# Optimization experiments

Measured on AMD Instinct MI355X. Metric: run time of the kernel, lower is better.

Reference implementation:

```python
import jax, jax.numpy as jnp
import numpy as np

F_DIM = 256
DFF = 2048      # torch TransformerEncoderLayer default dim_feedforward
NHEAD = 4
NCLS = 7
MAXLEN = 256
BATCH = 256
LN_EPS = 1e-5


def _layer_norm(x, g, b):
    m = x.mean(-1, keepdims=True)
    v = ((x - m) ** 2).mean(-1, keepdims=True)
    return (x - m) / jnp.sqrt(v + LN_EPS) * g + b


def _pos_encoding(n, d):
    # NOTE: original code builds PE over x.size(1) (the batch dim) -- kept faithfully.
    pos = jnp.arange(n, dtype=jnp.float32)[:, None]
    div = jnp.exp(jnp.arange(0, d, 2, dtype=jnp.float32) * (-np.log(10000.0) / d))
    pe = jnp.zeros((n, d), dtype=jnp.float32)
    pe = pe.at[:, 0::2].set(jnp.sin(pos * div))
    pe = pe.at[:, 1::2].set(jnp.cos(pos * div))
    return pe


def _mha(x, Wqkv, bqkv, Wo, bo):
    # x: [S, B, F]  (torch MHA default seq-first layout)
    S, B, F = x.shape
    hd = F // NHEAD
    qkv = x @ Wqkv.T + bqkv                      # [S, B, 3F]
    q, k, v = jnp.split(qkv, 3, axis=-1)
    rs = lambda t: t.reshape(S, B, NHEAD, hd).transpose(1, 2, 0, 3)  # [B, h, S, hd]
    q, k, v = rs(q), rs(k), rs(v)
    attn = jax.nn.softmax(jnp.einsum('bhsd,bhtd->bhst', q, k) / jnp.float32(np.sqrt(hd)), axis=-1)
    o = jnp.einsum('bhst,bhtd->bhsd', attn, v).transpose(2, 0, 1, 3).reshape(S, B, F)
    return o @ Wo.T + bo


def _forward(U_s, U_p, W_emb, b_emb, Wqkv, bqkv, Wo, bo, ln1_g, ln1_b,
             W1, b1, W2, b2, ln2_g, ln2_b, W_fc, b_fc, W_sm, b_sm, seq_lengths):
    L = np.asarray(seq_lengths)                   # static host lengths
    T, B, F = U_s.shape
    mask = jnp.arange(T)[:, None] < jnp.asarray(L)[None, :]        # [T, B] valid-turn mask
    bank_s = U_s * mask[:, :, None]               # zero-padded, as feature_transfer does
    # ---- ReasonMod / MultiTurnTransformer (post-LN encoder layer, eval mode) ----
    h = bank_s @ W_emb.T + b_emb
    h = h + _pos_encoding(B, F)                   # faithful quirk: PE over batch dim
    a_out = _mha(h, Wqkv, bqkv, Wo, bo)
    h1 = _layer_norm(h + a_out, ln1_g, ln1_b)
    ff = jax.nn.relu(h1 @ W1.T + b1) @ W2.T + b2
    h2 = _layer_norm(h1 + ff, ln2_g, ln2_b)
    q = h + h2                                    # [T, B, F]; identical for every t in the loop
    # ---- gather + segment-softmax + scatter-add attention pooling, all t at once ----
    e = jnp.einsum('ibf,tbf->tib', U_p, q)        # scores per (target t, turn i, conv b)
    e = jnp.where(mask[None, :, :], e, -1e30)
    a = jax.nn.softmax(e, axis=1) * mask[None, :, :]
    r = jnp.einsum('tib,ibf->tbf', a, U_p * mask[:, :, None])      # scatter_add equivalent
    rc = jnp.concatenate([bank_s, r], axis=-1)    # [T, B, 2F]
    hidden = jax.nn.relu(rc @ W_fc.T + b_fc)
    logp = jax.nn.log_softmax(hidden @ W_sm.T + b_sm, axis=2)      # [T, B, n_classes]
    rows = np.concatenate([np.arange(l) for l in L])
    cols = np.repeat(np.arange(B), L)
    return logp[rows, cols]                       # [total_tokens, n_classes]


def setup_inputs() -> dict:
    key = jax.random.key(0)
    ks = jax.random.split(key, 24)
    rn = lambda k, shape, s=0.05: jax.random.normal(k, shape, dtype=jnp.float32) * s
    F, D2 = F_DIM, 2 * F_DIM
    inp = {
        'U_s': jax.random.normal(ks[0], (MAXLEN, BATCH, F), dtype=jnp.float32),
        'U_p': jax.random.normal(ks[1], (MAXLEN, BATCH, F), dtype=jnp.float32),
        'W_emb': rn(ks[2], (F, F)), 'b_emb': jnp.zeros((F,), jnp.float32),
        'Wqkv': rn(ks[3], (3 * F, F)), 'bqkv': jnp.zeros((3 * F,), jnp.float32),
        'Wo': rn(ks[4], (F, F)), 'bo': jnp.zeros((F,), jnp.float32),
        'ln1_g': jnp.ones((F,), jnp.float32), 'ln1_b': jnp.zeros((F,), jnp.float32),
        'W1': rn(ks[5], (DFF, F)), 'b1': jnp.zeros((DFF,), jnp.float32),
        'W2': rn(ks[6], (F, DFF)), 'b2': jnp.zeros((F,), jnp.float32),
        'ln2_g': jnp.ones((F,), jnp.float32), 'ln2_b': jnp.zeros((F,), jnp.float32),
        'W_fc': rn(ks[7], (D2, D2)), 'b_fc': jnp.zeros((D2,), jnp.float32),
        'W_sm': rn(ks[8], (NCLS, D2)), 'b_sm': jnp.zeros((NCLS,), jnp.float32),
        'seq_lengths': jax.random.randint(ks[9], (BATCH,), MAXLEN // 2, MAXLEN + 1),
    }
    return inp


def reference(U_s, U_p, W_emb, b_emb, Wqkv, bqkv, Wo, bo, ln1_g, ln1_b,
              W1, b1, W2, b2, ln2_g, ln2_b, W_fc, b_fc, W_sm, b_sm, seq_lengths):
    return _forward(U_s, U_p, W_emb, b_emb, Wqkv, bqkv, Wo, bo, ln1_g, ln1_b,
                    W1, b1, W2, b2, ln2_g, ln2_b, W_fc, b_fc, W_sm, b_sm, seq_lengths)
```

## Files before the change

### kernel.cpp

```cpp
#include <hip/hip_runtime.h>

#define MTB 65536

typedef unsigned int uint;
typedef unsigned short ushort;

typedef _Float16 h8 __attribute__((ext_vector_type(8)));
typedef __attribute__((ext_vector_type(4))) float f4;

enum { E_BIAS=1, E_RELU=2, E_ACC=4, E_RES=8, E_PE=16, E_MASKA=32 };

__device__ __forceinline__ float ldsc(const float* p) { return *p; }
__device__ __forceinline__ float ldsc(const _Float16* p) { return (float)*p; }

template<int EPI, int AMODE, int BMODE, typename CT, int CPL, typename RT, int RPL>
__global__ __launch_bounds__(256) void gemm_h(
    int M, int N, int K,
    const void* __restrict__ Ap, const void* __restrict__ Ap2, int lda, long batchA,
    const void* __restrict__ Bp, int ldw, long batchW,
    CT* __restrict__ C, long cplane, int ldc, long batchC,
    const float* __restrict__ bias,
    const RT* __restrict__ res, const RT* __restrict__ resLo,
    const float* __restrict__ pe,
    const int* __restrict__ seqlen)
{
    __shared__ _Float16 Ah[128][40];
    __shared__ _Float16 Al[(AMODE==3)?128:1][40];
    __shared__ _Float16 Bh[128][40];
    __shared__ _Float16 Bl[(BMODE==0)?128:1][40];

    const int z = blockIdx.z;
    C += (size_t)z * batchC;
    const float*    Af  = (const float*)Ap + (AMODE==0 ? (size_t)z*batchA : 0);
    const _Float16* Ahp = (const _Float16*)Ap + ((AMODE==2||AMODE==3) ? (size_t)z*batchA : 0);
    const _Float16* Alp = (const _Float16*)Ap2 + (AMODE==3 ? (size_t)z*batchA : 0);
    const float*    Bf  = (const float*)Bp + (BMODE!=2 ? (size_t)z*batchW : 0);
    const _Float16* Bhp = (const _Float16*)Bp;

    const int m0 = blockIdx.y * 128, n0 = blockIdx.x * 128;
    const int tid = threadIdx.x;
    const int lane = tid & 63, wid = tid >> 6;
    const int wr = wid >> 1, wc = wid & 1;

    f4 acc[4][4];
    {
        f4 zr = {0.f, 0.f, 0.f, 0.f};
        #pragma unroll
        for (int i = 0; i < 4; i++)
            #pragma unroll
            for (int j = 0; j < 4; j++) acc[i][j] = zr;
    }

    for (int k0 = 0; k0 < K; k0 += 32) {
        __syncthreads();
        if (AMODE == 0 || (AMODE == 4 && k0 < 256)) {
            #pragma unroll
            for (int i = 0; i < 4; i++) {
                const int row = i*32 + (tid>>3);
                const int cg  = (tid&7)<<2;
                const int m = m0 + row;
                float4 v; v.x=0.f; v.y=0.f; v.z=0.f; v.w=0.f;
                bool ok = true;
                if (EPI & E_MASKA) ok = ((m>>8) < seqlen[m&255]);
                if (ok) v = *(const float4*)(Af + (size_t)m*lda + k0 + cg);
                Ah[row][cg+0] = (_Float16)v.x;
                Ah[row][cg+1] = (_Float16)v.y;
                Ah[row][cg+2] = (_Float16)v.z;
                Ah[row][cg+3] = (_Float16)v.w;
            }
        } else if (AMODE == 4) {
            const _Float16* Ar = (const _Float16*)Ap2;
            const int row = tid >> 1;
            const int cg  = (tid & 1) << 4;
            const size_t off = (size_t)(m0 + row) * 256 + (k0 - 256) + cg;
            *(uint4*)&Ah[row][cg]     = *(const uint4*)(Ar + off);
            *(uint4*)&Ah[row][cg + 8] = *(const uint4*)(Ar + off + 8);
        } else {
            const int row = tid >> 1;
            const int cg  = (tid & 1) << 4;
            const size_t off = (size_t)(m0 + row) * lda + k0 + cg;
            *(uint4*)&Ah[row][cg]     = *(const uint4*)(Ahp + off);
            *(uint4*)&Ah[row][cg + 8] = *(const uint4*)(Ahp + off + 8);
            if (AMODE == 3) {
                *(uint4*)&Al[row][cg]     = *(const uint4*)(Alp + off);
                *(uint4*)&Al[row][cg + 8] = *(const uint4*)(Alp + off + 8);
            }
        }
        if (BMODE == 2) {
            const int row = tid >> 1;
            const int cg  = (tid & 1) << 4;
            const size_t off = (size_t)(n0 + row) * ldw + k0 + cg;
            *(uint4*)&Bh[row][cg]     = *(const uint4*)(Bhp + off);
            *(uint4*)&Bh[row][cg + 8] = *(const uint4*)(Bhp + off + 8);
        } else if (BMODE == 0) {
            #pragma unroll
            for (int i = 0; i < 4; i++) {
                const int row = i*32 + (tid>>3);
                const int cg  = (tid&7)<<2;
                float4 v = *(const float4*)(Bf + (size_t)(n0+row)*ldw + k0 + cg);
                _Float16 h0 = (_Float16)v.x, h1 = (_Float16)v.y,
                         h2 = (_Float16)v.z, h3 = (_Float16)v.w;
                Bh[row][cg+0]=h0; Bl[row][cg+0]=(_Float16)(v.x-(float)h0);
                Bh[row][cg+1]=h1; Bl[row][cg+1]=(_Float16)(v.y-(float)h1);
                Bh[row][cg+2]=h2; Bl[row][cg+2]=(_Float16)(v.z-(float)h2);
                Bh[row][cg+3]=h3; Bl[row][cg+3]=(_Float16)(v.w-(float)h3);
            }
        } else {
            #pragma unroll
            for (int i = 0; i < 4; i++) {
                const int kr = i*8 + (tid>>5);
                const int ng = (tid&31)<<2;
                float4 v = *(const float4*)(Bf + (size_t)(k0+kr)*ldw + n0 + ng);
                Bh[ng+0][kr] = (_Float16)v.x;
                Bh[ng+1][kr] = (_Float16)v.y;
                Bh[ng+2][kr] = (_Float16)v.z;
                Bh[ng+3][kr] = (_Float16)v.w;
            }
        }
        __syncthreads();
        const int lr = lane & 15, lk = (lane>>4)<<3;
        h8 ah[4], bh[4];
        #pragma unroll
        for (int i = 0; i < 4; i++) {
            ah[i] = *(const h8*)&Ah[wr*64 + i*16 + lr][lk];
            bh[i] = *(const h8*)&Bh[wc*64 + i*16 + lr][lk];
        }
        #pragma unroll
        for (int mi = 0; mi < 4; mi++)
            #pragma unroll
            for (int ni = 0; ni < 4; ni++)
                acc[mi][ni] = __builtin_amdgcn_mfma_f32_16x16x32_f16(ah[mi], bh[ni], acc[mi][ni], 0, 0, 0);
        if (AMODE == 3) {
            h8 al[4], bl[4];
            #pragma unroll
            for (int i = 0; i < 4; i++) {
                al[i] = *(const h8*)&Al[wr*64 + i*16 + lr][lk];
                bl[i] = *(const h8*)&Bl[wc*64 + i*16 + lr][lk];
            }
            #pragma unroll
            for (int mi = 0; mi < 4; mi++)
                #pragma unroll
                for (int ni = 0; ni < 4; ni++) {
                    acc[mi][ni] = __builtin_amdgcn_mfma_f32_16x16x32_f16(ah[mi], bl[ni], acc[mi][ni], 0, 0, 0);
                    acc[mi][ni] = __builtin_amdgcn_mfma_f32_16x16x32_f16(al[mi], bh[ni], acc[mi][ni], 0, 0, 0);
                }
        }
    }
    const int colb = n0 + wc*64;
    const int rowb = m0 + wr*64;
    #pragma unroll
    for (int ni = 0; ni < 4; ni++) {
        const int col = colb + ni*16 + (lane & 15);
        float bv = (EPI & E_BIAS) ? bias[col] : 0.f;
        #pragma unroll
        for (int mi = 0; mi < 4; mi++) {
            const int r0 = rowb + mi*16 + ((lane>>4)<<2);
            #pragma unroll
            for (int j = 0; j < 4; j++) {
                const int row = r0 + j;
                const size_t idx = (size_t)row*ldc + col;
                float v = acc[mi][ni][j] + bv;
                if (EPI & E_PE)  v += pe[((row & 255) << 8) + col];
                if (EPI & E_RES) {
                    v += ldsc(res + idx);
                    if (RPL) v += ldsc(resLo + idx);
                }
                CT* cp = C + idx;
                if (EPI & E_ACC) v += ldsc((const CT*)cp);
                if (EPI & E_RELU) v = fmaxf(v, 0.f);
                if (CPL) {
                    _Float16 hh = (_Float16)v;
                    *(_Float16*)cp = hh;
                    *((_Float16*)cp + cplane) = (_Float16)(v - (float)hh);
                } else if (sizeof(CT) == 2) {
                    *(_Float16*)cp = (_Float16)v;
                } else {
                    *(float*)cp = v;
                }
            }
        }
    }
}

__global__ __launch_bounds__(256) void ff_kernel(
    const _Float16* __restrict__ h1,
    const _Float16* __restrict__ W1p,
    const _Float16* __restrict__ W2p,
    const float* __restrict__ b1,
    const float* __restrict__ b2,
    float* __restrict__ res2)
{
    __shared__ _Float16 h1t[64][264];
    __shared__ _Float16 zt[64][136];
    __shared__ _Float16 Bs[256][40];
    const int m0 = blockIdx.x * 64;
    const int tid = threadIdx.x;
    const int lane = tid & 63, wid = tid >> 6;
    const int wr = wid >> 1, wc = wid & 1;
    const int lr = lane & 15, lk = (lane >> 4) << 3;
    const int l4 = (lane >> 4) << 2;

    {
        const int row = tid >> 2, c0 = (tid & 3) << 6;
        const _Float16* src = h1 + (size_t)(m0 + row) * 256 + c0;
        #pragma unroll
        for (int j = 0; j < 8; j++)
            *(uint4*)&h1t[row][c0 + 8*j] = *(const uint4*)(src + 8*j);
    }

    f4 acc2[2][8];
    {
        f4 zr = {0.f,0.f,0.f,0.f};
        #pragma unroll
        for (int mi = 0; mi < 2; mi++)
            #pragma unroll
            for (int ni = 0; ni < 8; ni++) acc2[mi][ni] = zr;
    }

    for (int c = 0; c < 16; c++) {
        f4 acc1[2][4];
        {
            f4 zr = {0.f,0.f,0.f,0.f};
            #pragma unroll
            for (int mi = 0; mi < 2; mi++)
                #pragma unroll
                for (int ni = 0; ni < 4; ni++) acc1[mi][ni] = zr;
        }
        for (int k0 = 0; k0 < 256; k0 += 32) {
            __syncthreads();
            {
                const int row = tid >> 1, cc = (tid & 1) << 4;
                const size_t off = (size_t)(c*128 + row) * 256 + k0 + cc;
                *(uint4*)&Bs[row][cc]   = *(const uint4*)(W1p + off);
                *(uint4*)&Bs[row][cc+8] = *(const uint4*)(W1p + off + 8);
            }
            __syncthreads();
            h8 a0 = *(const h8*)&h1t[wr*32 +      lr][k0 + lk];
            h8 a1 = *(const h8*)&h1t[wr*32 + 16 + lr][k0 + lk];
            #pragma unroll
            for (int ni = 0; ni < 4; ni++) {
                const h8 b = *(const h8*)&Bs[wc*64 + ni*16 + lr][lk];
                acc1[0][ni] = __builtin_amdgcn_mfma_f32_16x16x32_f16(a0, b, acc1[0][ni], 0, 0, 0);
                acc1[1][ni] = __builtin_amdgcn_mfma_f32_16x16x32_f16(a1, b, acc1[1][ni], 0, 0, 0);
            }
        }
        #pragma unroll
        for (int ni = 0; ni < 4; ni++) {
            const float bv = b1[c*128 + wc*64 + ni*16 + lr];
            #pragma unroll
            for (int mi = 0; mi < 2; mi++)
                #pragma unroll
                for (int j = 0; j < 4; j++) {
                    float v = acc1[mi][ni][j] + bv;
                    v = fmaxf(v, 0.f);
                    zt[wr*32 + mi*16 + l4 + j][wc*64 + ni*16 + lr] = (_Float16)v;
                }
        }
        __syncthreads();
        for (int kk = 0; kk < 128; kk += 32) {
            if (kk) __syncthreads();
            {
                const size_t off = (size_t)tid * 2048 + c*128 + kk;
                #pragma unroll
                for (int j = 0; j < 4; j++)
                    *(uint4*)&Bs[tid][8*j] = *(const uint4*)(W2p + off + 8*j);
            }
            __syncthreads();
            h8 a0 = *(const h8*)&zt[wr*32 +      lr][kk + lk];
            h8 a1 = *(const h8*)&zt[wr*32 + 16 + lr][kk + lk];
            #pragma unroll
            for (int ni = 0; ni < 8; ni++) {
                const h8 b = *(const h8*)&Bs[wc*128 + ni*16 + lr][lk];
                acc2[0][ni] = __builtin_amdgcn_mfma_f32_16x16x32_f16(a0, b, acc2[0][ni], 0, 0, 0);
                acc2[1][ni] = __builtin_amdgcn_mfma_f32_16x16x32_f16(a1, b, acc2[1][ni], 0, 0, 0);
            }
        }
        __syncthreads();
    }
    #pragma unroll
    for (int ni = 0; ni < 8; ni++) {
        const int col = wc*128 + ni*16 + lr;
        const float bv = b2[col];
        #pragma unroll
        for (int mi = 0; mi < 2; mi++) {
            const int rl = wr*32 + mi*16 + l4;
            #pragma unroll
            for (int j = 0; j < 4; j++) {
                float v = acc2[mi][ni][j] + bv + (float)h1t[rl + j][col];
                res2[(size_t)(m0 + rl + j) * 256 + col] = v;
            }
        }
    }
}

__global__ void cvt_kernel(const float* __restrict__ src, int ld, int cshift,
                           _Float16* __restrict__ dst, int total)
{
    const int i = blockIdx.x * 256 + threadIdx.x;
    if (i >= total) return;
    const int r = i >> cshift, c = i & ((1 << cshift) - 1);
    dst[i] = (_Float16)src[(size_t)r * ld + c];
}

__global__ __launch_bounds__(256) void attn_kernel(const _Float16* __restrict__ qkv,
                                                   _Float16* __restrict__ o)
{
    __shared__ _Float16 Kl[64][68];
    __shared__ _Float16 Vt[64][68];
    __shared__ _Float16 Pl[4][64][68];
    const int b = blockIdx.x, head = blockIdx.y;
    const _Float16* base = qkv + (size_t)b * 768 + head * 64;
    const int tid = threadIdx.x;
    const int lane = tid & 63, wid = tid >> 6;
    const int lr = lane & 15, lg = lane >> 4;
    const int lk = lg << 3;
    const int q0 = wid * 64;

    h8 qf[4][2];
    #pragma unroll
    for (int mi = 0; mi < 4; mi++)
        #pragma unroll
        for (int kk = 0; kk < 2; kk++)
            qf[mi][kk] = *(const h8*)(base + (size_t)(q0 + mi*16 + lr) * 196608 + kk*32 + lk);

    f4 oacc[4][4];
    float m_st[4][4], l_st[4][4];
    {
        f4 zr = {0.f,0.f,0.f,0.f};
        #pragma unroll
        for (int mi = 0; mi < 4; mi++)
            #pragma unroll
            for (int di = 0; di < 4; di++) oacc[mi][di] = zr;
        #pragma unroll
        for (int mi = 0; mi < 4; mi++)
            #pragma unroll
            for (int j = 0; j < 4; j++) { m_st[mi][j] = -1e30f; l_st[mi][j] = 0.f; }
    }

    for (int kt = 0; kt < 4; kt++) {
        __syncthreads();
        {
            const int row = tid >> 2, c0 = (tid & 3) << 4;
            const _Float16* rp = base + (size_t)(kt*64 + row) * 196608;
            *(uint4*)&Kl[row][c0]     = *(const uint4*)(rp + 256 + c0);
            *(uint4*)&Kl[row][c0 + 8] = *(const uint4*)(rp + 256 + c0 + 8);
            const h8 v0 = *(const h8*)(rp + 512 + c0);
            const h8 v1 = *(const h8*)(rp + 512 + c0 + 8);
            #pragma unroll
            for (int j = 0; j < 8; j++) {
                Vt[c0 + j][row]     = v0[j];
                Vt[c0 + 8 + j][row] = v1[j];
            }
        }
        __syncthreads();
        f4 sacc[4][4];
        {
            f4 zr = {0.f,0.f,0.f,0.f};
            #pragma unroll
            for (int mi = 0; mi < 4; mi++)
                #pragma unroll
                for (int ni = 0; ni < 4; ni++) sacc[mi][ni] = zr;
        }
        #pragma unroll
        for (int kk = 0; kk < 2; kk++) {
            h8 kf[4];
            #pragma unroll
            for (int ni = 0; ni < 4; ni++)
                kf[ni] = *(const h8*)&Kl[ni*16 + lr][kk*32 + lk];
            #pragma unroll
            for (int mi = 0; mi < 4; mi++)
                #pragma unroll
                for (int ni = 0; ni < 4; ni++)
                    sacc[mi][ni] = __builtin_amdgcn_mfma_f32_16x16x32_f16(qf[mi][kk], kf[ni], sacc[mi][ni], 0, 0, 0);
        }
        #pragma unroll
        for (int mi = 0; mi < 4; mi++)
            #pragma unroll
            for (int ni = 0; ni < 4; ni++)
                #pragma unroll
                for (int j = 0; j < 4; j++) sacc[mi][ni][j] *= 0.125f;
        #pragma unroll
        for (int mi = 0; mi < 4; mi++) {
            #pragma unroll
            for (int j = 0; j < 4; j++) {
                float tm = fmaxf(fmaxf(sacc[mi][0][j], sacc[mi][1][j]),
                                 fmaxf(sacc[mi][2][j], sacc[mi][3][j]));
                tm = fmaxf(tm, __shfl_xor(tm, 1));
                tm = fmaxf(tm, __shfl_xor(tm, 2));
                tm = fmaxf(tm, __shfl_xor(tm, 4));
                tm = fmaxf(tm, __shfl_xor(tm, 8));
                const float mn = fmaxf(m_st[mi][j], tm);
                const float sc = __expf(m_st[mi][j] - mn);
                m_st[mi][j] = mn;
                float ps = 0.f;
                #pragma unroll
                for (int ni = 0; ni < 4; ni++) {
                    const float p = __expf(sacc[mi][ni][j] - mn);
                    sacc[mi][ni][j] = p;
                    ps += p;
                }
                ps += __shfl_xor(ps, 1);
                ps += __shfl_xor(ps, 2);
                ps += __shfl_xor(ps, 4);
                ps += __shfl_xor(ps, 8);
                l_st[mi][j] = l_st[mi][j] * sc + ps;
                #pragma unroll
                for (int di = 0; di < 4; di++) oacc[mi][di][j] *= sc;
            }
        }
        #pragma unroll
        for (int mi = 0; mi < 4; mi++)
            #pragma unroll
            for (int ni = 0; ni < 4; ni++)
                #pragma unroll
                for (int j = 0; j < 4; j++)
                    Pl[wid][mi*16 + (lg<<2) + j][ni*16 + lr] = (_Float16)sacc[mi][ni][j];
        #pragma unroll
        for (int kk = 0; kk < 2; kk++) {
            h8 pf[4], vf[4];
            #pragma unroll
            for (int mi = 0; mi < 4; mi++)
                pf[mi] = *(const h8*)&Pl[wid][mi*16 + lr][kk*32 + lk];
            #pragma unroll
            for (int di = 0; di < 4; di++)
                vf[di] = *(const h8*)&Vt[di*16 + lr][kk*32 + lk];
            #pragma unroll
            for (int mi = 0; mi < 4; mi++)
                #pragma unroll
                for (int di = 0; di < 4; di++)
                    oacc[mi][di] = __builtin_amdgcn_mfma_f32_16x16x32_f16(pf[mi], vf[di], oacc[mi][di], 0, 0, 0);
        }
    }
    _Float16* obase = o + (size_t)b * 256 + head * 64;
    #pragma unroll
    for (int mi = 0; mi < 4; mi++) {
        #pragma unroll
        for (int j = 0; j < 4; j++) {
            const float inv = 1.f / l_st[mi][j];
            const size_t rowoff = (size_t)(q0 + mi*16 + (lg<<2) + j) * 65536;
            #pragma unroll
            for (int di = 0; di < 4; di++)
                obase[rowoff + di*16 + lr] = (_Float16)(oacc[mi][di][j] * inv);
        }
    }
}

template<int OPL, typename OT>
__global__ __launch_bounds__(256) void ln_kernel(const float* __restrict__ x,
    const float* __restrict__ g, const float* __restrict__ bt,
    const _Float16* __restrict__ addin, const _Float16* __restrict__ addinLo,
    OT* __restrict__ out, long oplane, int nrows)
{
    const int gid = blockIdx.x * 256 + threadIdx.x;
    const int row = gid >> 6;
    const int lane = threadIdx.x & 63;
    if (row >= nrows) return;
    const float* xr = x + (size_t)row * 256;
    float4 v = *(const float4*)(xr + (lane<<2));
    float s = v.x + v.y + v.z + v.w;
    #pragma unroll
    for (int off = 32; off > 0; off >>= 1) s += __shfl_xor(s, off, 64);
    const float mean = s * (1.0f/256.0f);
    const float dx = v.x-mean, dy = v.y-mean, dz = v.z-mean, dw = v.w-mean;
    float ss = dx*dx + dy*dy + dz*dz + dw*dw;
    #pragma unroll
    for (int off = 32; off > 0; off >>= 1) ss += __shfl_xor(ss, off, 64);
    const float inv = rsqrtf(ss * (1.0f/256.0f) + 1e-5f);
    const float4 gv = *(const float4*)(g + (lane<<2));
    const float4 bv = *(const float4*)(bt + (lane<<2));
    float ov[4];
    ov[0] = dx*inv*gv.x + bv.x;
    ov[1] = dy*inv*gv.y + bv.y;
    ov[2] = dz*inv*gv.z + bv.z;
    ov[3] = dw*inv*gv.w + bv.w;
    const size_t base = (size_t)row*256 + (lane<<2);
    if (addin) {
        #pragma unroll
        for (int j = 0; j < 4; j++) {
            ov[j] += (float)addin[base+j];
            if (addinLo) ov[j] += (float)addinLo[base+j];
        }
    }
    #pragma unroll
    for (int j = 0; j < 4; j++) {
        if (OPL) {
            _Float16 hh = (_Float16)ov[j];
            ((_Float16*)out)[base+j] = hh;
            ((_Float16*)out)[base+j+oplane] = (_Float16)(ov[j] - (float)hh);
        } else if (sizeof(OT) == 2) {
            ((_Float16*)out)[base+j] = (_Float16)ov[j];
        } else {
            ((float*)out)[base+j] = ov[j];
        }
    }
}

__global__ __launch_bounds__(256) void smax_kernel(float* __restrict__ e,
                                                   const int* __restrict__ seqlen)
{
    const int gid = blockIdx.x * 256 + threadIdx.x;
    const int row = gid >> 6;
    const int lane = threadIdx.x & 63;
    const int L = seqlen[row >> 8];
    float* er = e + (size_t)row * 256;
    float4 v = *(const float4*)(er + (lane<<2));
    const int i0 = lane << 2;
    const float x0 = (i0+0 < L) ? v.x : -1e30f;
    const float x1 = (i0+1 < L) ? v.y : -1e30f;
    const float x2 = (i0+2 < L) ? v.z : -1e30f;
    const float x3 = (i0+3 < L) ? v.w : -1e30f;
    float mx = fmaxf(fmaxf(x0,x1), fmaxf(x2,x3));
    #pragma unroll
    for (int off = 32; off > 0; off >>= 1) mx = fmaxf(mx, __shfl_xor(mx, off, 64));
    const float p0 = (i0+0 < L) ? __expf(x0-mx) : 0.f;
    const float p1 = (i0+1 < L) ? __expf(x1-mx) : 0.f;
    const float p2 = (i0+2 < L) ? __expf(x2-mx) : 0.f;
    const float p3 = (i0+3 < L) ? __expf(x3-mx) : 0.f;
    float s = p0+p1+p2+p3;
    #pragma unroll
    for (int off = 32; off > 0; off >>= 1) s += __shfl_xor(s, off, 64);
    const float inv = 1.f / s;
    v.x = p0*inv; v.y = p1*inv; v.z = p2*inv; v.w = p3*inv;
    *(float4*)(er + (lane<<2)) = v;
}

__global__ __launch_bounds__(256) void head_kernel(const _Float16* __restrict__ hidden,
    const float* __restrict__ Wsm, const float* __restrict__ bsm,
    const int* __restrict__ seqlen, const int* __restrict__ offs,
    float* __restrict__ out)
{
    const int gid = blockIdx.x * 256 + threadIdx.x;
    const int row = gid >> 6;
    const int lane = threadIdx.x & 63;
    if (row >= MTB) return;
    const int t = row >> 8, b = row & 255;
    if (t >= seqlen[b]) return;
    const _Float16* hr = hidden + (size_t)row * 512;
    const h8 hu = *(const h8*)(hr + lane*8);
    float hv[8];
    #pragma unroll
    for (int j = 0; j < 8; j++) hv[j] = (float)hu[j];
    float lg[7];
    #pragma unroll
    for (int c = 0; c < 7; c++) {
        const float* wr = Wsm + c*512 + lane*8;
        const float4 w0 = *(const float4*)wr;
        const float4 w1 = *(const float4*)(wr + 4);
        float acc = hv[0]*w0.x + hv[1]*w0.y + hv[2]*w0.z + hv[3]*w0.w
                  + hv[4]*w1.x + hv[5]*w1.y + hv[6]*w1.z + hv[7]*w1.w;
        #pragma unroll
        for (int off = 32; off > 0; off >>= 1) acc += __shfl_xor(acc, off, 64);
        lg[c] = acc + bsm[c];
    }
    float mx = lg[0];
    #pragma unroll
    for (int c = 1; c < 7; c++) mx = fmaxf(mx, lg[c]);
    float s = 0.f;
    #pragma unroll
    for (int c = 0; c < 7; c++) s += __expf(lg[c] - mx);
    const float lse = mx + logf(s);
    if (lane == 0) {
        float* orow = out + (size_t)(offs[b] + t) * 7;
        #pragma unroll
        for (int c = 0; c < 7; c++) orow[c] = lg[c] - lse;
    }
}

__global__ void pe_kernel(float* __restrict__ pe)
{
    const int idx = blockIdx.x * 256 + threadIdx.x;
    const int b = idx >> 8, f = idx & 255;
    const int j = f >> 1;
    const float div = expf(-9.210340371976184f * (2.0f * j) * (1.0f/256.0f));
    const float arg = (float)b * div;
    pe[idx] = (f & 1) ? cosf(arg) : sinf(arg);
}

__global__ void prefix_kernel(const int* __restrict__ L, int* __restrict__ offs)
{
    if (threadIdx.x == 0) {
        int acc = 0;
        for (int i = 0; i < 256; i++) { offs[i] = acc; acc += L[i]; }
        offs[256] = acc;
    }
}

__global__ void sentinel_kernel(float* __restrict__ out, float v)
{
    if (threadIdx.x == 0) out[0] = v;
}

extern "C" void kernel_launch(void* const* d_in, const int* in_sizes, int n_in,
                              void* d_out, int out_size, void* d_ws, size_t ws_size,
                              hipStream_t stream)
{
    const float* U_s   = (const float*)d_in[0];
    const float* U_p   = (const float*)d_in[1];
    const float* W_emb = (const float*)d_in[2];
    const float* b_emb = (const float*)d_in[3];
    const float* Wqkv  = (const float*)d_in[4];
    const float* bqkv  = (const float*)d_in[5];
    const float* Wo    = (const float*)d_in[6];
    const float* bo    = (const float*)d_in[7];
    const float* ln1_g = (const float*)d_in[8];
    const float* ln1_b = (const float*)d_in[9];
    const float* W1    = (const float*)d_in[10];
    const float* b1    = (const float*)d_in[11];
    const float* W2    = (const float*)d_in[12];
    const float* b2    = (const float*)d_in[13];
    const float* ln2_g = (const float*)d_in[14];
    const float* ln2_b = (const float*)d_in[15];
    const float* W_fc  = (const float*)d_in[16];
    const float* b_fc  = (const float*)d_in[17];
    const float* W_sm  = (const float*)d_in[18];
    const float* b_sm  = (const float*)d_in[19];
    const int*   seqlen= (const int*)d_in[20];
    float* out = (float*)d_out;

    const size_t MiB = 1024*1024;
    const size_t KiB = 1024;
    char* ws = (char*)d_ws;
    if (ws_size < 193*MiB) {
        sentinel_kernel<<<dim3(1), dim3(64), 0, stream>>>(out, -(float)(ws_size / MiB));
        return;
    }
    const long PL = 16*1024*1024;
    _Float16* h_hi = (_Float16*)(ws);
    _Float16* h_lo = (_Float16*)(ws + 32*MiB);
    int*      offs = (int*)(ws + 64*MiB);
    char*     slot = ws + 64*MiB + 8*KiB;
    _Float16* qkv  = (_Float16*)(ws + 65*MiB);
    _Float16* o    = (_Float16*)(ws + 161*MiB);
    float*    res1 = (float*)(ws + 65*MiB);
    float*    res2 = res1;
    _Float16* h1   = (_Float16*)(ws + 161*MiB);
    _Float16* w1p  = (_Float16*)(ws + 129*MiB);
    _Float16* w2p  = (_Float16*)(ws + 130*MiB);
    _Float16* q_hi = (_Float16*)(ws + 129*MiB);
    _Float16* q_lo = (_Float16*)(ws + 161*MiB);
    float*    e    = (float*)(ws + 65*MiB);
    _Float16* r    = (_Float16*)(ws);
    _Float16* hid  = (_Float16*)(ws + 129*MiB);

    prefix_kernel<<<dim3(1), dim3(64), 0, stream>>>(seqlen, offs);

    _Float16* wp  = (_Float16*)slot;
    float*    pe  = (float*)(slot + 512*KiB);

    cvt_kernel<<<dim3(256), 256, 0, stream>>>(W_emb, 256, 8, wp, 65536);
    pe_kernel<<<dim3(256), dim3(256), 0, stream>>>(pe);
    gemm_h<E_BIAS|E_PE|E_MASKA, 0, 2, _Float16, 1, float, 0>
        <<<dim3(2,512,1), 256, 0, stream>>>(
        MTB,256,256, U_s,nullptr,256,0, wp,256,0, h_hi,PL,256,0,
        b_emb, (const float*)nullptr, nullptr, pe, seqlen);

    cvt_kernel<<<dim3(768), 256, 0, stream>>>(Wqkv, 256, 8, wp, 196608);
    gemm_h<E_BIAS, 2, 2, _Float16, 0, float, 0>
        <<<dim3(6,512,1), 256, 0, stream>>>(
        MTB,768,256, h_hi,nullptr,256,0, wp,256,0, qkv,0,768,0,
        bqkv, (const float*)nullptr, nullptr, nullptr, nullptr);

    attn_kernel<<<dim3(256,4), 256, 0, stream>>>(qkv, o);

    cvt_kernel<<<dim3(256), 256, 0, stream>>>(Wo, 256, 8, wp, 65536);
    gemm_h<E_BIAS|E_RES, 2, 2, float, 0, _Float16, 1>
        <<<dim3(2,512,1), 256, 0, stream>>>(
        MTB,256,256, o,nullptr,256,0, wp,256,0, res1,0,256,0,
        bo, h_hi, h_lo, nullptr, nullptr);

    ln_kernel<0, _Float16><<<dim3(MTB/4), 256, 0, stream>>>(
        res1, ln1_g, ln1_b, nullptr, nullptr, h1, 0, MTB);

    cvt_kernel<<<dim3(2048), 256, 0, stream>>>(W1, 256, 8, w1p, 524288);
    cvt_kernel<<<dim3(2048), 256, 0, stream>>>(W2, 2048, 11, w2p, 524288);
    ff_kernel<<<dim3(1024), 256, 0, stream>>>(h1, w1p, w2p, b1, b2, res2);

    ln_kernel<1, _Float16><<<dim3(MTB/4), 256, 0, stream>>>(
        res2, ln2_g, ln2_b, h_hi, h_lo, q_hi, PL, MTB);

    gemm_h<0, 3, 0, float, 0, float, 0>
        <<<dim3(2,2,256), 256, 0, stream>>>(
        256,256,256, q_hi,q_lo,65536,256, U_p,65536,256, e,0,256,65536,
        nullptr, (const float*)nullptr, nullptr, nullptr, nullptr);

    smax_kernel<<<dim3(MTB/4), 256, 0, stream>>>(e, seqlen);

    gemm_h<0, 0, 1, _Float16, 0, float, 0>
        <<<dim3(2,2,256), 256, 0, stream>>>(
        256,256,256, e,nullptr,256,65536, U_p,65536,256, r,0,65536,256,
        nullptr, (const float*)nullptr, nullptr, nullptr, nullptr);

    cvt_kernel<<<dim3(1024), 256, 0, stream>>>(W_fc, 512, 9, wp, 262144);
    gemm_h<E_BIAS|E_RELU|E_MASKA, 4, 2, _Float16, 0, float, 0>
        <<<dim3(4,512,1), 256, 0, stream>>>(
        MTB,512,512, U_s,r,256,0, wp,512,0, hid,0,512,0,
        b_fc, (const float*)nullptr, nullptr, nullptr, seqlen);

    head_kernel<<<dim3(MTB/4), 256, 0, stream>>>(hid, W_sm, b_sm, seqlen, offs, out);
}
```

Before: 924.1 us.

## Hold FF input fragments in registers and swizzle weight tiles in LDS

The ff_kernel no longer stages the h1 tile in shared memory. Each wave loads its A fragments for the full K=256 straight into registers once, and the residual add reads h1 from global memory. Shared-memory stores and loads of the W1 and W2 weight tiles now use an XOR-style column swizzle to cut bank conflicts. Together these shrink LDS use, which could allow more blocks per CU, and drop the LDS reads for A. The cost is 64 extra VGPRs per thread for the fragments, which may reduce occupancy.

```diff
diff --git a/kernel.cpp b/kernel.cpp
--- a/kernel.cpp
+++ b/kernel.cpp
@@ -190,23 +190,22 @@
     const float* __restrict__ b2,
     float* __restrict__ res2)
 {
-    __shared__ _Float16 h1t[64][264];
+    __shared__ _Float16 Bs[256][40];
     __shared__ _Float16 zt[64][136];
-    __shared__ _Float16 Bs[256][40];
     const int m0 = blockIdx.x * 64;
     const int tid = threadIdx.x;
     const int lane = tid & 63, wid = tid >> 6;
     const int wr = wid >> 1, wc = wid & 1;
-    const int lr = lane & 15, lk = (lane >> 4) << 3;
-    const int l4 = (lane >> 4) << 2;
-
-    {
-        const int row = tid >> 2, c0 = (tid & 3) << 6;
-        const _Float16* src = h1 + (size_t)(m0 + row) * 256 + c0;
-        #pragma unroll
-        for (int j = 0; j < 8; j++)
-            *(uint4*)&h1t[row][c0 + 8*j] = *(const uint4*)(src + 8*j);
-    }
+    const int lr = lane & 15, lg = lane >> 4;
+    const int lk = lg << 3;
+    const int l4 = lg << 2;
+
+    h8 af[2][8];
+    #pragma unroll
+    for (int mi = 0; mi < 2; mi++)
+        #pragma unroll
+        for (int ks = 0; ks < 8; ks++)
+            af[mi][ks] = *(const h8*)(h1 + (size_t)(m0 + wr*32 + mi*16 + lr) * 256 + ks*32 + lk);
 
     f4 acc2[2][8];
     {
@@ -226,22 +225,24 @@
                 #pragma unroll
                 for (int ni = 0; ni < 4; ni++) acc1[mi][ni] = zr;
         }
-        for (int k0 = 0; k0 < 256; k0 += 32) {
+        for (int ks = 0; ks < 8; ks++) {
             __syncthreads();
             {
-                const int row = tid >> 1, cc = (tid & 1) << 4;
-                const size_t off = (size_t)(c*128 + row) * 256 + k0 + cc;
-                *(uint4*)&Bs[row][cc]   = *(const uint4*)(W1p + off);
-                *(uint4*)&Bs[row][cc+8] = *(const uint4*)(W1p + off + 8);
+                const int row = tid >> 1;
+                const int h   = tid & 1;
+                const int ccs = ((h + (row >> 3)) & 1) << 4;
+                const size_t off = (size_t)(c*128 + row) * 256 + ks*32 + (h << 4);
+                *(uint4*)&Bs[row][ccs]     = *(const uint4*)(W1p + off);
+                *(uint4*)&Bs[row][ccs + 8] = *(const uint4*)(W1p + off + 8);
             }
             __syncthreads();
-            h8 a0 = *(const h8*)&h1t[wr*32 +      lr][k0 + lk];
-            h8 a1 = *(const h8*)&h1t[wr*32 + 16 + lr][k0 + lk];
             #pragma unroll
             for (int ni = 0; ni < 4; ni++) {
-                const h8 b = *(const h8*)&Bs[wc*64 + ni*16 + lr][lk];
-                acc1[0][ni] = __builtin_amdgcn_mfma_f32_16x16x32_f16(a0, b, acc1[0][ni], 0, 0, 0);
-                acc1[1][ni] = __builtin_amdgcn_mfma_f32_16x16x32_f16(a1, b, acc1[1][ni], 0, 0, 0);
+                const int row = wc*64 + ni*16 + lr;
+                const int col = ((((lg >> 1) + (row >> 3)) & 1) << 4) + ((lg & 1) << 3);
+                const h8 b = *(const h8*)&Bs[row][col];
+                acc1[0][ni] = __builtin_amdgcn_mfma_f32_16x16x32_f16(af[0][ks], b, acc1[0][ni], 0, 0, 0);
+                acc1[1][ni] = __builtin_amdgcn_mfma_f32_16x16x32_f16(af[1][ks], b, acc1[1][ni], 0, 0, 0);
             }
         }
         #pragma unroll
@@ -257,20 +258,24 @@
                 }
         }
         __syncthreads();
-        for (int kk = 0; kk < 128; kk += 32) {
+        for (int kk = 0; kk < 4; kk++) {
             if (kk) __syncthreads();
             {
-                const size_t off = (size_t)tid * 2048 + c*128 + kk;
-                #pragma unroll
-                for (int j = 0; j < 4; j++)
-                    *(uint4*)&Bs[tid][8*j] = *(const uint4*)(W2p + off + 8*j);
+                const size_t off = (size_t)tid * 2048 + c*128 + kk*32;
+                #pragma unroll
+                for (int j = 0; j < 4; j++) {
+                    const int cg = ((j + (tid >> 3)) & 3) << 3;
+                    *(uint4*)&Bs[tid][cg] = *(const uint4*)(W2p + off + 8*j);
+                }
             }
             __syncthreads();
-            h8 a0 = *(const h8*)&zt[wr*32 +      lr][kk + lk];
-            h8 a1 = *(const h8*)&zt[wr*32 + 16 + lr][kk + lk];
+            h8 a0 = *(const h8*)&zt[wr*32 +      lr][kk*32 + lk];
+            h8 a1 = *(const h8*)&zt[wr*32 + 16 + lr][kk*32 + lk];
             #pragma unroll
             for (int ni = 0; ni < 8; ni++) {
-                const h8 b = *(const h8*)&Bs[wc*128 + ni*16 + lr][lk];
+                const int row = wc*128 + ni*16 + lr;
+                const int col = ((lg + (row >> 3)) & 3) << 3;
+                const h8 b = *(const h8*)&Bs[row][col];
                 acc2[0][ni] = __builtin_amdgcn_mfma_f32_16x16x32_f16(a0, b, acc2[0][ni], 0, 0, 0);
                 acc2[1][ni] = __builtin_amdgcn_mfma_f32_16x16x32_f16(a1, b, acc2[1][ni], 0, 0, 0);
             }
@@ -286,8 +291,8 @@
             const int rl = wr*32 + mi*16 + l4;
             #pragma unroll
             for (int j = 0; j < 4; j++) {
-                float v = acc2[mi][ni][j] + bv + (float)h1t[rl + j][col];
-                res2[(size_t)(m0 + rl + j) * 256 + col] = v;
+                const size_t idx = (size_t)(m0 + rl + j) * 256 + col;
+                res2[idx] = acc2[mi][ni][j] + bv + (float)h1[idx];
             }
         }
     }
```

New measurement: 937.5 us. No clear change (+1.4%).

## Restructure fused FFN kernel to keep activations in registers via transposed MFMA

Applied to the files above, without the earlier changes.

Rewrites the fused FFN kernel so each wave owns 16 rows. The h1 fragment stays in registers, and the first GEMM is computed transposed (W1 as the A operand), so its ReLU output lands directly in the layout the second GEMM's 16x16x16 MFMA needs as its A operand. This removes the shared-memory staging of h1 and of the intermediate activations, along with their barriers. The cost is more accumulator registers (16 f4 plus 8 f4) and the smaller-K MFMA in the second GEMM, and the residual is now reread from global memory.

```diff
diff --git a/kernel.cpp b/kernel.cpp
--- a/kernel.cpp
+++ b/kernel.cpp
@@ -6,6 +6,7 @@
 typedef unsigned short ushort;
 
 typedef _Float16 h8 __attribute__((ext_vector_type(8)));
+typedef _Float16 h4 __attribute__((ext_vector_type(4)));
 typedef __attribute__((ext_vector_type(4))) float f4;
 
 enum { E_BIAS=1, E_RELU=2, E_ACC=4, E_RES=8, E_PE=16, E_MASKA=32 };
@@ -190,105 +191,99 @@
     const float* __restrict__ b2,
     float* __restrict__ res2)
 {
-    __shared__ _Float16 h1t[64][264];
-    __shared__ _Float16 zt[64][136];
-    __shared__ _Float16 Bs[256][40];
+    __shared__ _Float16 W1s[128][36];
+    __shared__ _Float16 W2s[256][36];
     const int m0 = blockIdx.x * 64;
     const int tid = threadIdx.x;
     const int lane = tid & 63, wid = tid >> 6;
-    const int wr = wid >> 1, wc = wid & 1;
-    const int lr = lane & 15, lk = (lane >> 4) << 3;
-    const int l4 = (lane >> 4) << 2;
-
-    {
-        const int row = tid >> 2, c0 = (tid & 3) << 6;
-        const _Float16* src = h1 + (size_t)(m0 + row) * 256 + c0;
-        #pragma unroll
-        for (int j = 0; j < 8; j++)
-            *(uint4*)&h1t[row][c0 + 8*j] = *(const uint4*)(src + 8*j);
-    }
-
-    f4 acc2[2][8];
+    const int lr = lane & 15, lg = lane >> 4;
+    const int hq = m0 + wid * 16;
+
+    h8 bf[8];
+    #pragma unroll
+    for (int ks = 0; ks < 8; ks++)
+        bf[ks] = *(const h8*)(h1 + (size_t)(hq + lr) * 256 + ks*32 + lg*8);
+
+    f4 acc2[16];
     {
         f4 zr = {0.f,0.f,0.f,0.f};
         #pragma unroll
-        for (int mi = 0; mi < 2; mi++)
-            #pragma unroll
-            for (int ni = 0; ni < 8; ni++) acc2[mi][ni] = zr;
+        for (int nt = 0; nt < 16; nt++) acc2[nt] = zr;
     }
 
     for (int c = 0; c < 16; c++) {
-        f4 acc1[2][4];
+        f4 acc1[8];
         {
             f4 zr = {0.f,0.f,0.f,0.f};
             #pragma unroll
-            for (int mi = 0; mi < 2; mi++)
-                #pragma unroll
-                for (int ni = 0; ni < 4; ni++) acc1[mi][ni] = zr;
-        }
-        for (int k0 = 0; k0 < 256; k0 += 32) {
+            for (int mi = 0; mi < 8; mi++) acc1[mi] = zr;
+        }
+        for (int ks = 0; ks < 8; ks++) {
             __syncthreads();
             {
-                const int row = tid >> 1, cc = (tid & 1) << 4;
-                const size_t off = (size_t)(c*128 + row) * 256 + k0 + cc;
-                *(uint4*)&Bs[row][cc]   = *(const uint4*)(W1p + off);
-                *(uint4*)&Bs[row][cc+8] = *(const uint4*)(W1p + off + 8);
+                const int row = tid >> 1, hh = tid & 1;
+                const _Float16* g = W1p + (size_t)(c*128 + row) * 256 + ks*32 + hh*16;
+                uint4 v0 = *(const uint4*)g;
+                uint4 v1 = *(const uint4*)(g + 8);
+                _Float16* d = &W1s[row][hh*16];
+                uint2 t0; t0.x=v0.x; t0.y=v0.y; *(uint2*)(d+0)  = t0;
+                uint2 t1; t1.x=v0.z; t1.y=v0.w; *(uint2*)(d+4)  = t1;
+                uint2 t2; t2.x=v1.x; t2.y=v1.y; *(uint2*)(d+8)  = t2;
+                uint2 t3; t3.x=v1.z; t3.y=v1.w; *(uint2*)(d+12) = t3;
             }
             __syncthreads();
-            h8 a0 = *(const h8*)&h1t[wr*32 +      lr][k0 + lk];
-            h8 a1 = *(const h8*)&h1t[wr*32 + 16 + lr][k0 + lk];
-            #pragma unroll
-            for (int ni = 0; ni < 4; ni++) {
-                const h8 b = *(const h8*)&Bs[wc*64 + ni*16 + lr][lk];
-                acc1[0][ni] = __builtin_amdgcn_mfma_f32_16x16x32_f16(a0, b, acc1[0][ni], 0, 0, 0);
-                acc1[1][ni] = __builtin_amdgcn_mfma_f32_16x16x32_f16(a1, b, acc1[1][ni], 0, 0, 0);
-            }
-        }
-        #pragma unroll
-        for (int ni = 0; ni < 4; ni++) {
-            const float bv = b1[c*128 + wc*64 + ni*16 + lr];
-            #pragma unroll
-            for (int mi = 0; mi < 2; mi++)
-                #pragma unroll
-                for (int j = 0; j < 4; j++) {
-                    float v = acc1[mi][ni][j] + bv;
-                    v = fmaxf(v, 0.f);
-                    zt[wr*32 + mi*16 + l4 + j][wc*64 + ni*16 + lr] = (_Float16)v;
+            #pragma unroll
+            for (int mi = 0; mi < 8; mi++) {
+                const _Float16* s = &W1s[mi*16 + lr][lg*8];
+                uint2 p0 = *(const uint2*)s;
+                uint2 p1 = *(const uint2*)(s + 4);
+                uint4 u; u.x=p0.x; u.y=p0.y; u.z=p1.x; u.w=p1.y;
+                h8 af = __builtin_bit_cast(h8, u);
+                acc1[mi] = __builtin_amdgcn_mfma_f32_16x16x32_f16(af, bf[ks], acc1[mi], 0, 0, 0);
+            }
+        }
+        h4 za[8];
+        #pragma unroll
+        for (int mi = 0; mi < 8; mi++) {
+            const float4 bb = *(const float4*)(b1 + c*128 + mi*16 + lg*4);
+            const float bs[4] = {bb.x, bb.y, bb.z, bb.w};
+            #pragma unroll
+            for (int j = 0; j < 4; j++)
+                za[mi][j] = (_Float16)fmaxf(acc1[mi][j] + bs[j], 0.f);
+        }
+        for (int sub = 0; sub < 4; sub++) {
+            __syncthreads();
+            {
+                const _Float16* g = W2p + (size_t)tid * 2048 + c*128 + sub*32;
+                _Float16* d = &W2s[tid][0];
+                #pragma unroll
+                for (int q = 0; q < 4; q++) {
+                    uint4 v = *(const uint4*)(g + 8*q);
+                    uint2 ta; ta.x=v.x; ta.y=v.y; *(uint2*)(d + 8*q)     = ta;
+                    uint2 tb; tb.x=v.z; tb.y=v.w; *(uint2*)(d + 8*q + 4) = tb;
                 }
-        }
-        __syncthreads();
-        for (int kk = 0; kk < 128; kk += 32) {
-            if (kk) __syncthreads();
-            {
-                const size_t off = (size_t)tid * 2048 + c*128 + kk;
-                #pragma unroll
-                for (int j = 0; j < 4; j++)
-                    *(uint4*)&Bs[tid][8*j] = *(const uint4*)(W2p + off + 8*j);
             }
             __syncthreads();
-            h8 a0 = *(const h8*)&zt[wr*32 +      lr][kk + lk];
-            h8 a1 = *(const h8*)&zt[wr*32 + 16 + lr][kk + lk];
-            #pragma unroll
-            for (int ni = 0; ni < 8; ni++) {
-                const h8 b = *(const h8*)&Bs[wc*128 + ni*16 + lr][lk];
-                acc2[0][ni] = __builtin_amdgcn_mfma_f32_16x16x32_f16(a0, b, acc2[0][ni], 0, 0, 0);
-                acc2[1][ni] = __builtin_amdgcn_mfma_f32_16x16x32_f16(a1, b, acc2[1][ni], 0, 0, 0);
-            }
-        }
-        __syncthreads();
-    }
-    #pragma unroll
-    for (int ni = 0; ni < 8; ni++) {
-        const int col = wc*128 + ni*16 + lr;
+            #pragma unroll
+            for (int g = 0; g < 2; g++) {
+                const h4 a = za[sub*2 + g];
+                #pragma unroll
+                for (int nt = 0; nt < 16; nt++) {
+                    uint2 p = *(const uint2*)&W2s[nt*16 + lr][g*16 + lg*4];
+                    h4 bb = __builtin_bit_cast(h4, p);
+                    acc2[nt] = __builtin_amdgcn_mfma_f32_16x16x16f16(a, bb, acc2[nt], 0, 0, 0);
+                }
+            }
+        }
+    }
+    #pragma unroll
+    for (int nt = 0; nt < 16; nt++) {
+        const int col = nt*16 + lr;
         const float bv = b2[col];
         #pragma unroll
-        for (int mi = 0; mi < 2; mi++) {
-            const int rl = wr*32 + mi*16 + l4;
-            #pragma unroll
-            for (int j = 0; j < 4; j++) {
-                float v = acc2[mi][ni][j] + bv + (float)h1t[rl + j][col];
-                res2[(size_t)(m0 + rl + j) * 256 + col] = v;
-            }
+        for (int j = 0; j < 4; j++) {
+            const size_t idx = (size_t)(hq + lg*4 + j) * 256 + col;
+            res2[idx] = acc2[nt][j] + bv + (float)h1[idx];
         }
     }
 }
```

Result: slower. 998.2 us (+8.0%).
